# Optimization experiments

Measured on AMD Instinct MI355X. Metric: run time of the kernel, lower is better.

Reference implementation:

```python
import jax, jax.numpy as jnp
import numpy as np

NUM_HEAD = 16
D_Q = 512
D_KV = 512
ROPE_BASE = 10000.0


def _cos_sin(seq_len, dim):
    # Replicates calculate_cos_sin: theta = base**(-2*ids) / (dim//2)
    pos = jnp.arange(seq_len, dtype=jnp.float32)[:, None]          # (S,1)
    ids = jnp.arange(dim // 2, dtype=jnp.float32)                  # (D/2,)
    theta = (ROPE_BASE ** (-2.0 * ids)) / (dim // 2)
    r = pos * theta[None, :]                                       # (S, D/2)
    return jnp.cos(r), jnp.sin(r)


def _rope(x, cos, sin):
    b, s, d = x.shape
    xv = x.reshape(b, s, d // 2, 2)
    x0, x1 = xv[..., 0], xv[..., 1]
    out = jnp.stack([x0 * cos - x1 * sin, x1 * cos + x0 * sin], axis=-1)
    return out.reshape(b, s, d)


def setup_inputs() -> dict:
    key = jax.random.key(0)
    ks = jax.random.split(key, 10)
    d_model, d_q, d_kv = 1024, D_Q, D_KV
    b, s = 2, 2048
    w = lambda k, i, o: jax.random.normal(k, (i, o), dtype=jnp.float32) * 0.02
    return {
        "x": jax.random.normal(ks[0], (b, s, d_model), dtype=jnp.float32),
        "Wd_q_w": w(ks[1], d_model, d_q), "Wd_q_b": jnp.zeros((d_q,), jnp.float32),
        "Wu_q_w": w(ks[2], d_q, d_model), "Wu_q_b": jnp.zeros((d_model,), jnp.float32),
        "Wq_r_w": w(ks[3], d_q, d_model), "Wq_r_b": jnp.zeros((d_model,), jnp.float32),
        "Wk_r_w": w(ks[4], d_model, d_model), "Wk_r_b": jnp.zeros((d_model,), jnp.float32),
        "Wd_kv_w": w(ks[5], d_model, d_kv), "Wd_kv_b": jnp.zeros((d_kv,), jnp.float32),
        "Wu_k_w": w(ks[6], d_kv, d_model), "Wu_k_b": jnp.zeros((d_model,), jnp.float32),
        "Wu_v_w": w(ks[7], d_kv, d_model), "Wu_v_b": jnp.zeros((d_model,), jnp.float32),
        "Wo_w": w(ks[8], d_model, d_model), "Wo_b": jnp.zeros((d_model,), jnp.float32),
    }


def reference(x, Wd_q_w, Wd_q_b, Wu_q_w, Wu_q_b, Wq_r_w, Wq_r_b,
              Wk_r_w, Wk_r_b, Wd_kv_w, Wd_kv_b, Wu_k_w, Wu_k_b,
              Wu_v_w, Wu_v_b, Wo_w, Wo_b):
    b, s, d_model = x.shape
    h = NUM_HEAD
    hd = d_model // h
    scale = jnp.sqrt(jnp.float32(h + D_KV + D_Q))

    def heads(t):  # (b,s,d) -> (b,h,s,hd)
        return t.reshape(b, s, h, hd).transpose(0, 2, 1, 3)

    cos, sin = _cos_sin(s, d_model)

    ct_q = x @ Wd_q_w + Wd_q_b                                   # (b,s,d_q)
    qt_c = heads(ct_q @ Wu_q_w + Wu_q_b)
    qt_r = heads(_rope(ct_q @ Wq_r_w + Wq_r_b, cos, sin))
    query = qt_c + qt_r                                          # (b,h,s,hd)

    ct_kv = x @ Wd_kv_w + Wd_kv_b                                # (b,s,d_kv)
    kt_c = heads(ct_kv @ Wu_k_w + Wu_k_b)
    kt_r = heads(_rope(x @ Wk_r_w + Wk_r_b, cos, sin))
    key = kt_c + kt_r
    value = heads(ct_kv @ Wu_v_w + Wu_v_b)

    attn = jnp.einsum('bhqd,bhkd->bhqk', query, key) / scale
    attn = jax.nn.softmax(attn, axis=-1)
    out = jnp.einsum('bhqk,bhkd->bhqd', attn, value)
    out = out.transpose(0, 2, 1, 3).reshape(b, s, d_model)
    return out @ Wo_w + Wo_b
```

## Files before the change

### kernel.cpp

```cpp
#include <hip/hip_runtime.h>
#include <hip/hip_bf16.h>
#include <math.h>
#include <limits.h>

typedef __hip_bfloat16 bf16;
typedef __bf16 bf16x8 __attribute__((ext_vector_type(8)));
typedef float  f32x4  __attribute__((ext_vector_type(4)));

#define DEVI __device__ __forceinline__

static constexpr int Bb     = 2;
static constexpr int Ss     = 2048;
static constexpr int DMODEL = 1024;
static constexpr int NTOK   = Bb * Ss;

DEVI float bf2f(bf16 v) { return __bfloat162float(v); }
DEVI bf16  f2bf(float v) { return __float2bfloat16(v); }

DEVI unsigned int packbf(float lo, float hi) {
  union { bf16 b; unsigned short u; } a, c;
  a.b = f2bf(lo); c.b = f2bf(hi);
  return ((unsigned int)c.u << 16) | a.u;
}
DEVI float bfu2f(unsigned short u) {
  unsigned int x = (unsigned int)u << 16;
  float f; __builtin_memcpy(&f, &x, 4); return f;
}

DEVI void async_load16(const bf16* g, bf16* l) {
  __builtin_amdgcn_global_load_lds((const __attribute__((address_space(1))) void*)g,
                                   (__attribute__((address_space(3))) void*)l, 16, 0, 0);
}

__global__ __launch_bounds__(256) void convert_kernel(
    const float* __restrict__ in, bf16* __restrict__ out, int n4) {
  const int t = blockIdx.x * blockDim.x + threadIdx.x;
  if (t >= n4) return;
  const float4 v = ((const float4*)in)[t];
  uint2 o; o.x = packbf(v.x, v.y); o.y = packbf(v.z, v.w);
  *(uint2*)&out[(size_t)t * 4] = o;
}

struct TransDesc { const float* src; bf16* dst; int R; int C; int tstart; };
struct TransPack { TransDesc d[8]; };

__global__ __launch_bounds__(256) void transpose8_kernel(TransPack p) {
  const int t = blockIdx.x;
  int i = 0;
#pragma unroll
  for (int j = 1; j < 8; ++j) if (t >= p.d[j].tstart) i = j;
  const float* __restrict__ in = p.d[i].src;
  bf16* __restrict__ out = p.d[i].dst;
  const int R = p.d[i].R, C = p.d[i].C;
  const int rel = t - p.d[i].tstart;
  const int tilesC = C >> 6;
  const int r0 = (rel / tilesC) * 64, c0 = (rel % tilesC) * 64;

  __shared__ bf16 tl[64][65];
  const int tc = threadIdx.x & 63, tr = threadIdx.x >> 6;
#pragma unroll
  for (int q = 0; q < 16; ++q) {
    int r = tr + q * 4;
    tl[r][tc] = f2bf(in[(size_t)(r0 + r) * C + c0 + tc]);
  }
  __syncthreads();
#pragma unroll
  for (int q = 0; q < 16; ++q) {
    int r = tr + q * 4;
    out[(size_t)(c0 + r) * R + r0 + tc] = tl[tc][r];
  }
}

struct GemmDesc {
  const bf16* A; const bf16* WT; const float* b1; const float* b2; bf16* C;
  int lda, ldb, ldc, K, bsplit, nTX, blkStart, biasRow;
};
struct GemmBatch { GemmDesc d[4]; };

__global__ __launch_bounds__(256) void gemm_batch_kernel(GemmBatch gb) {
  const int t = blockIdx.x;
  int di = 0;
#pragma unroll
  for (int j = 1; j < 4; ++j) if (t >= gb.d[j].blkStart) di = j;
  const GemmDesc D = gb.d[di];
  const int rel = t - D.blkStart;
  const int tileN = (rel % D.nTX) * 128;
  const int tileM = (rel / D.nTX) * 128;

  __shared__ bf16 ldsA[128 * 32];
  __shared__ bf16 ldsB[128 * 32];
  const int tid = threadIdx.x;
  const int lane = tid & 63;
  const int w = tid >> 6;
  const int wr = w >> 1, wc = w & 1;
  const int l15 = lane & 15, lg = lane >> 4;
  const int lrow = lane >> 2;
  const int lcol = (lane & 3) * 8;

  f32x4 acc[4][4] = {};

  for (int k0 = 0; k0 < D.K; k0 += 32) {
    async_load16(D.A  + (size_t)(tileM + w * 32 +      lrow) * D.lda + k0 + lcol, &ldsA[(w * 32) * 32]);
    async_load16(D.A  + (size_t)(tileM + w * 32 + 16 + lrow) * D.lda + k0 + lcol, &ldsA[(w * 32 + 16) * 32]);
    async_load16(D.WT + (size_t)(tileN + w * 32 +      lrow) * D.ldb + k0 + lcol, &ldsB[(w * 32) * 32]);
    async_load16(D.WT + (size_t)(tileN + w * 32 + 16 + lrow) * D.ldb + k0 + lcol, &ldsB[(w * 32 + 16) * 32]);
    __syncthreads();

    bf16x8 af[4], bfr[4];
#pragma unroll
    for (int i = 0; i < 4; ++i) {
      af[i]  = *(const bf16x8*)&ldsA[(wr * 64 + i * 16 + l15) * 32 + lg * 8];
      bfr[i] = *(const bf16x8*)&ldsB[(wc * 64 + i * 16 + l15) * 32 + lg * 8];
    }
#pragma unroll
    for (int i = 0; i < 4; ++i)
#pragma unroll
      for (int j = 0; j < 4; ++j)
        acc[i][j] = __builtin_amdgcn_mfma_f32_16x16x32_bf16(af[i], bfr[j], acc[i][j], 0, 0, 0);
    __syncthreads();
  }

  const int mbase = tileM + wr * 64;
  const int nbase = tileN + wc * 64;
#pragma unroll
  for (int j = 0; j < 4; ++j) {
    int col = nbase + j * 16 + l15;
    float bvc = D.biasRow ? 0.0f : (col < D.bsplit ? D.b1[col] : D.b2[col - D.bsplit]);
#pragma unroll
    for (int i = 0; i < 4; ++i)
#pragma unroll
      for (int r = 0; r < 4; ++r) {
        int row = mbase + i * 16 + lg * 4 + r;
        float bv = D.biasRow ? D.b1[row] : bvc;
        D.C[(size_t)row * D.ldc + col] = f2bf(acc[i][j][r] + bv);
      }
  }
}

__global__ __launch_bounds__(256) void gemm_kernel_f32(
    const bf16* __restrict__ A, int lda,
    const bf16* __restrict__ WT, int ldb,
    const float* __restrict__ b1,
    float* __restrict__ Cout, int ldc, int K) {
  __shared__ bf16 ldsA[128 * 32];
  __shared__ bf16 ldsB[128 * 32];
  const int tid = threadIdx.x;
  const int lane = tid & 63;
  const int w = tid >> 6;
  const int wr = w >> 1, wc = w & 1;
  const int tileM = blockIdx.y * 128;
  const int tileN = blockIdx.x * 128;
  const int l15 = lane & 15, lg = lane >> 4;
  const int lrow = lane >> 2;
  const int lcol = (lane & 3) * 8;

  f32x4 acc[4][4] = {};

  for (int k0 = 0; k0 < K; k0 += 32) {
    async_load16(A  + (size_t)(tileM + w * 32 +      lrow) * lda + k0 + lcol, &ldsA[(w * 32) * 32]);
    async_load16(A  + (size_t)(tileM + w * 32 + 16 + lrow) * lda + k0 + lcol, &ldsA[(w * 32 + 16) * 32]);
    async_load16(WT + (size_t)(tileN + w * 32 +      lrow) * ldb + k0 + lcol, &ldsB[(w * 32) * 32]);
    async_load16(WT + (size_t)(tileN + w * 32 + 16 + lrow) * ldb + k0 + lcol, &ldsB[(w * 32 + 16) * 32]);
    __syncthreads();

    bf16x8 af[4], bfr[4];
#pragma unroll
    for (int i = 0; i < 4; ++i) {
      af[i]  = *(const bf16x8*)&ldsA[(wr * 64 + i * 16 + l15) * 32 + lg * 8];
      bfr[i] = *(const bf16x8*)&ldsB[(wc * 64 + i * 16 + l15) * 32 + lg * 8];
    }
#pragma unroll
    for (int i = 0; i < 4; ++i)
#pragma unroll
      for (int j = 0; j < 4; ++j)
        acc[i][j] = __builtin_amdgcn_mfma_f32_16x16x32_bf16(af[i], bfr[j], acc[i][j], 0, 0, 0);
    __syncthreads();
  }

  const int mbase = tileM + wr * 64;
  const int nbase = tileN + wc * 64;
#pragma unroll
  for (int j = 0; j < 4; ++j) {
    int col = nbase + j * 16 + l15;
    float bvc = b1[col];
#pragma unroll
    for (int i = 0; i < 4; ++i)
#pragma unroll
      for (int r = 0; r < 4; ++r) {
        int row = mbase + i * 16 + lg * 4 + r;
        Cout[(size_t)row * ldc + col] = acc[i][j][r] + bvc;
      }
  }
}

__global__ __launch_bounds__(256) void combine_rope_kernel(
    const bf16* __restrict__ Gc, int ldc_,
    const bf16* __restrict__ Gr, int ldr_,
    bf16* __restrict__ out) {
  const int t = blockIdx.x * blockDim.x + threadIdx.x;
  const int g = t & 127, row = t >> 7;
  const int s = row & (Ss - 1);
  union { bf16x8 v; unsigned short u[8]; } vc, vr;
  vc.v = *(const bf16x8*)&Gc[(size_t)row * ldc_ + (size_t)g * 8];
  vr.v = *(const bf16x8*)&Gr[(size_t)row * ldr_ + (size_t)g * 8];
  uint4 o;
  unsigned int* op = &o.x;
#pragma unroll
  for (int qq = 0; qq < 4; ++qq) {
    const int p = g * 4 + qq;
    float c, sn;
    if (p == 0) {
      float rr = (float)s * (1.0f / 512.0f);
      c = cosf(rr); sn = sinf(rr);
    } else {
      float theta = exp2f(-26.5754247590989f * (float)p) * (1.0f / 512.0f);
      sn = (float)s * theta; c = 1.0f;
    }
    float g0 = bfu2f(vr.u[2 * qq]), g1 = bfu2f(vr.u[2 * qq + 1]);
    float c0 = bfu2f(vc.u[2 * qq]), c1 = bfu2f(vc.u[2 * qq + 1]);
    op[qq] = packbf(c0 + g0 * c - g1 * sn, c1 + g1 * c + g0 * sn);
  }
  *(uint4*)&out[(size_t)row * DMODEL + (size_t)g * 8] = o;
}

__global__ __launch_bounds__(256) void attn_kernel(
    const bf16* __restrict__ Qn, const bf16* __restrict__ Kn,
    const bf16* __restrict__ VT, bf16* __restrict__ AO) {
  const int bh = blockIdx.x, qt = blockIdx.y;
  const int b = bh >> 4, h = bh & 15;
  const int tid = threadIdx.x, lane = tid & 63, w = tid >> 6;
  const int q0 = qt * 64 + w * 16;
  const int l15 = lane & 15, lg = lane >> 4;
  const float SC2 = 0.044736075f;
  const float THR = 11.5415603f;

  __shared__ bf16 ldsK[2][64 * 64];
  __shared__ bf16 ldsV[2][64 * 64];
  __shared__ bf16 ldsP[4][16 * 64];

  const bf16* Kg = Kn + (size_t)(b * Ss) * DMODEL + h * 64;
  const bf16* Vg = VT + (size_t)(h * 64) * NTOK + b * Ss;

  const int r0 = tid >> 3;
  const int srcb = ((tid & 7) * 16) ^ ((r0 & 7) << 4);
  const char* kS0 = (const char*)(Kg + (size_t)r0 * DMODEL) + srcb;
  const char* kS1 = (const char*)(Kg + (size_t)(32 + r0) * DMODEL) + srcb;
  const char* vS0 = (const char*)(Vg + (size_t)r0 * NTOK) + srcb;
  const char* vS1 = (const char*)(Vg + (size_t)(32 + r0) * NTOK) + srcb;
  const ptrdiff_t kAdv = (ptrdiff_t)64 * DMODEL * 2;
  const ptrdiff_t vAdv = 128;

  bf16* kd0_b0 = &ldsK[0][w * 512]; bf16* kd1_b0 = &ldsK[0][2048 + w * 512];
  bf16* kd0_b1 = &ldsK[1][w * 512]; bf16* kd1_b1 = &ldsK[1][2048 + w * 512];
  bf16* vd0_b0 = &ldsV[0][w * 512]; bf16* vd1_b0 = &ldsV[0][2048 + w * 512];
  bf16* vd0_b1 = &ldsV[1][w * 512]; bf16* vd1_b1 = &ldsV[1][2048 + w * 512];

  auto stageTo = [&](bf16* kd0, bf16* kd1, bf16* vd0, bf16* vd1) {
    async_load16((const bf16*)kS0, kd0);
    async_load16((const bf16*)kS1, kd1);
    async_load16((const bf16*)vS0, vd0);
    async_load16((const bf16*)vS1, vd1);
    kS0 += kAdv; kS1 += kAdv; vS0 += vAdv; vS1 += vAdv;
  };

  const int kswz = (l15 & 7) << 4;
  const int xA = (lg * 16) ^ kswz;
  const int xB = (64 + lg * 16) ^ kswz;
  const char* krA0 = (const char*)&ldsK[0][0] + l15 * 128 + xA;
  const char* krB0 = (const char*)&ldsK[0][0] + l15 * 128 + xB;
  const char* krA1 = (const char*)&ldsK[1][0] + l15 * 128 + xA;
  const char* krB1 = (const char*)&ldsK[1][0] + l15 * 128 + xB;
  const char* vrA0 = (const char*)&ldsV[0][0] + l15 * 128 + xA;
  const char* vrB0 = (const char*)&ldsV[0][0] + l15 * 128 + xB;
  const char* vrA1 = (const char*)&ldsV[1][0] + l15 * 128 + xA;
  const char* vrB1 = (const char*)&ldsV[1][0] + l15 * 128 + xB;

  char* Pw = (char*)&ldsP[w][0];
  char* pwr[4];
#pragma unroll
  for (int j = 0; j < 4; ++j) {
    const int chunk = (j * 2 + (lg >> 1)) ^ (l15 & 7);
    pwr[j] = Pw + l15 * 128 + chunk * 16 + (lg & 1) * 8;
  }
  const char* paA = Pw + l15 * 128 + xA;
  const char* paB = Pw + l15 * 128 + xB;

  const bf16* Qbase = Qn + (size_t)(b * Ss + q0 + l15) * DMODEL + h * 64;
  bf16x8 bq0 = *(const bf16x8*)&Qbase[lg * 8];
  bf16x8 bq1 = *(const bf16x8*)&Qbase[32 + lg * 8];

  float m = 0.0f, l = 0.0f;
  f32x4 accO[4] = {};

  auto body = [&](const char* krA, const char* krB, const char* vrA, const char* vrB) {
    f32x4 sa[4] = {};
#pragma unroll
    for (int j = 0; j < 4; ++j) {
      bf16x8 ak0 = *(const bf16x8*)(krA + j * 2048);
      bf16x8 ak1 = *(const bf16x8*)(krB + j * 2048);
      sa[j] = __builtin_amdgcn_mfma_f32_16x16x32_bf16(ak0, bq0, sa[j], 0, 0, 0);
      sa[j] = __builtin_amdgcn_mfma_f32_16x16x32_bf16(ak1, bq1, sa[j], 0, 0, 0);
    }
    float pmaxr = -3.0e38f;
#pragma unroll
    for (int j = 0; j < 4; ++j)
#pragma unroll
      for (int r = 0; r < 4; ++r) pmaxr = fmaxf(pmaxr, sa[j][r]);
    if (__any(fmaf(pmaxr, SC2, -m) > THR)) {
      float px = fmaxf(pmaxr, __shfl_xor(pmaxr, 16, 64));
      px = fmaxf(px, __shfl_xor(px, 32, 64));
      float mnew = fmaxf(m, px * SC2);
      float corr = __builtin_amdgcn_exp2f(m - mnew);
      m = mnew; l *= corr;
      float cr[4];
#pragma unroll
      for (int r = 0; r < 4; ++r) cr[r] = __shfl(corr, lg * 4 + r, 64);
#pragma unroll
      for (int dj = 0; dj < 4; ++dj)
#pragma unroll
        for (int r = 0; r < 4; ++r) accO[dj][r] *= cr[r];
    }
    float p[4][4];
    float ts0 = 0.f, ts1 = 0.f;
#pragma unroll
    for (int j = 0; j < 4; ++j) {
#pragma unroll
      for (int r = 0; r < 4; ++r)
        p[j][r] = __builtin_amdgcn_exp2f(fmaf(sa[j][r], SC2, -m));
      ts0 += p[j][0] + p[j][2];
      ts1 += p[j][1] + p[j][3];
    }
    float ts = ts0 + ts1;
    ts += __shfl_xor(ts, 16, 64);
    ts += __shfl_xor(ts, 32, 64);
    l += ts;
#pragma unroll
    for (int j = 0; j < 4; ++j) {
      uint2 pw;
      pw.x = packbf(p[j][0], p[j][1]);
      pw.y = packbf(p[j][2], p[j][3]);
      *(uint2*)pwr[j] = pw;
    }
    bf16x8 pa0 = *(const bf16x8*)paA;
    bf16x8 pa1 = *(const bf16x8*)paB;
#pragma unroll
    for (int dj = 0; dj < 4; ++dj) {
      bf16x8 bv0 = *(const bf16x8*)(vrA + dj * 2048);
      bf16x8 bv1 = *(const bf16x8*)(vrB + dj * 2048);
      accO[dj] = __builtin_amdgcn_mfma_f32_16x16x32_bf16(pa0, bv0, accO[dj], 0, 0, 0);
      accO[dj] = __builtin_amdgcn_mfma_f32_16x16x32_bf16(pa1, bv1, accO[dj], 0, 0, 0);
    }
  };

  stageTo(kd0_b0, kd1_b0, vd0_b0, vd1_b0);
  for (int tt = 0; tt < 16; ++tt) {
    __syncthreads();
    stageTo(kd0_b1, kd1_b1, vd0_b1, vd1_b1);
    body(krA0, krB0, vrA0, vrB0);
    __syncthreads();
    if (tt < 15) stageTo(kd0_b0, kd1_b0, vd0_b0, vd1_b0);
    body(krA1, krB1, vrA1, vrB1);
  }

  float linv[4];
#pragma unroll
  for (int r = 0; r < 4; ++r) linv[r] = 1.0f / __shfl(l, lg * 4 + r, 64);
#pragma unroll
  for (int dj = 0; dj < 4; ++dj)
#pragma unroll
    for (int r = 0; r < 4; ++r)
      AO[(size_t)(b * Ss + q0 + lg * 4 + r) * DMODEL + h * 64 + dj * 16 + l15] =
          f2bf(accO[dj][r] * linv[r]);
}

extern "C" void kernel_launch(void* const* d_in, const int* in_sizes, int n_in,
                              void* d_out, int out_size, void* d_ws, size_t ws_size,
                              hipStream_t stream) {
  const float* x      = (const float*)d_in[0];
  const float* Wdq    = (const float*)d_in[1];  const float* Wdq_b  = (const float*)d_in[2];
  const float* Wuq    = (const float*)d_in[3];  const float* Wuq_b  = (const float*)d_in[4];
  const float* Wqr    = (const float*)d_in[5];  const float* Wqr_b  = (const float*)d_in[6];
  const float* Wkr    = (const float*)d_in[7];  const float* Wkr_b  = (const float*)d_in[8];
  const float* Wdkv   = (const float*)d_in[9];  const float* Wdkv_b = (const float*)d_in[10];
  const float* Wuk    = (const float*)d_in[11]; const float* Wuk_b  = (const float*)d_in[12];
  const float* Wuv    = (const float*)d_in[13]; const float* Wuv_b  = (const float*)d_in[14];
  const float* Wo     = (const float*)d_in[15]; const float* Wo_b   = (const float*)d_in[16];

  char* ws = (char*)d_ws;
  size_t off = 0;
  bf16* WdqT   = (bf16*)(ws + off); off += (size_t)512  * 1024 * 2;
  bf16* WdkvT  = (bf16*)(ws + off); off += (size_t)512  * 1024 * 2;
  bf16* WuqT   = (bf16*)(ws + off); off += (size_t)1024 * 512  * 2;
  bf16* WqrT   = (bf16*)(ws + off); off += (size_t)1024 * 512  * 2;
  bf16* WukT   = (bf16*)(ws + off); off += (size_t)1024 * 512  * 2;
  bf16* WuvT   = (bf16*)(ws + off); off += (size_t)1024 * 512  * 2;
  bf16* WkrT   = (bf16*)(ws + off); off += (size_t)1024 * 1024 * 2;
  bf16* WoT    = (bf16*)(ws + off); off += (size_t)1024 * 1024 * 2;
  bf16* x_bf   = (bf16*)(ws + off); off += (size_t)NTOK * 1024 * 2;
  bf16* ct     = (bf16*)(ws + off); off += (size_t)NTOK * 1024 * 2;
  bf16* Ga     = (bf16*)(ws + off); off += (size_t)NTOK * 1024 * 2;
  bf16* VTr    = (bf16*)(ws + off); off += (size_t)NTOK * 1024 * 2;
  bf16* Gupk   = x_bf;
  bf16* Qn     = (bf16*)d_out;
  bf16* Kn     = (bf16*)d_out + (size_t)NTOK * DMODEL;
  bf16* AO     = Ga;
  (void)ws_size; (void)in_sizes; (void)n_in; (void)out_size;

  TransPack tp = {{
    { Wdq,  WdqT,  1024, 512,  0    },
    { Wdkv, WdkvT, 1024, 512,  128  },
    { Wuq,  WuqT,  512,  1024, 256  },
    { Wqr,  WqrT,  512,  1024, 384  },
    { Wuk,  WukT,  512,  1024, 512  },
    { Wuv,  WuvT,  512,  1024, 640  },
    { Wkr,  WkrT,  1024, 1024, 768  },
    { Wo,   WoT,   1024, 1024, 1024 },
  }};
  transpose8_kernel<<<1280, 256, 0, stream>>>(tp);
  convert_kernel<<<(NTOK * DMODEL / 4 + 255) / 256, 256, 0, stream>>>(x, x_bf, NTOK * DMODEL / 4);

  GemmBatch ba = {{
    { x_bf, WdqT, Wdq_b, Wdkv_b, ct, 1024, 1024, 1024, 1024, 512,     8, 0,       0 },
    { x_bf, WkrT, Wkr_b, Wkr_b,  Kn, 1024, 1024, 1024, 1024, INT_MAX, 8, 256,     0 },
    { 0, 0, 0, 0, 0, 0, 0, 0, 0, 0, 1, INT_MAX, 0 },
    { 0, 0, 0, 0, 0, 0, 0, 0, 0, 0, 1, INT_MAX, 0 },
  }};
  gemm_batch_kernel<<<512, 256, 0, stream>>>(ba);

  GemmBatch bb = {{
    { ct,       WuqT,     Wuq_b, Wuq_b, Ga,   1024, 512,  1024, 512, INT_MAX, 8,  0,   0 },
    { ct,       WqrT,     Wqr_b, Wqr_b, Qn,   1024, 512,  1024, 512, INT_MAX, 8,  256, 0 },
    { ct + 512, WukT,     Wuk_b, Wuk_b, Gupk, 1024, 512,  1024, 512, INT_MAX, 8,  512, 0 },
    { WuvT,     ct + 512, Wuv_b, Wuv_b, VTr,  512,  1024, NTOK, 512, INT_MAX, 32, 768, 1 },
  }};
  gemm_batch_kernel<<<1024, 256, 0, stream>>>(bb);

  combine_rope_kernel<<<NTOK * 128 / 256, 256, 0, stream>>>(Ga, 1024, Qn, 1024, Qn);
  combine_rope_kernel<<<NTOK * 128 / 256, 256, 0, stream>>>(Gupk, 1024, Kn, 1024, Kn);

  attn_kernel<<<dim3(32, 32), 256, 0, stream>>>(Qn, Kn, VTr, AO);

  gemm_kernel_f32<<<dim3(8, 32), 256, 0, stream>>>(
      AO, 1024, WoT, 1024, Wo_b, (float*)d_out, 1024, 1024);
}
```

Before: 197.4 us.

## Precompose low-rank projection weights and replace RoPE combine with rank-2 fixup

The down- and up-projections are multiplied together on device into full 1024x1024 matrices, and their biases are folded in. Q, K and V then each come from a single GEMM on x, replacing the two-stage low-rank chain and the separate x@Wkr GEMM. K's rotary term is added through a new addend path in the GEMM epilogue. The elementwise combine/RoPE passes are replaced by a small fixup kernel that only corrects the first rotary pair, since the other frequencies are negligible. This cuts main-GEMM FLOPs and intermediate traffic, at the cost of extra weight-composition GEMMs, a prep kernel and different bf16 rounding paths.

After: 297.7 us. +50.8%, slower.

```diff
diff --git a/kernel.cpp b/kernel.cpp
--- a/kernel.cpp
+++ b/kernel.cpp
@@ -22,26 +22,28 @@
   a.b = f2bf(lo); c.b = f2bf(hi);
   return ((unsigned int)c.u << 16) | a.u;
 }
-DEVI float bfu2f(unsigned short u) {
-  unsigned int x = (unsigned int)u << 16;
-  float f; __builtin_memcpy(&f, &x, 4); return f;
-}
 
 DEVI void async_load16(const bf16* g, bf16* l) {
   __builtin_amdgcn_global_load_lds((const __attribute__((address_space(1))) void*)g,
                                    (__attribute__((address_space(3))) void*)l, 16, 0, 0);
 }
 
-__global__ __launch_bounds__(256) void convert_kernel(
-    const float* __restrict__ in, bf16* __restrict__ out, int n4) {
-  const int t = blockIdx.x * blockDim.x + threadIdx.x;
-  if (t >= n4) return;
+__global__ __launch_bounds__(256) void convert3_kernel(
+    const float* __restrict__ i0, bf16* __restrict__ o0, int n0,
+    const float* __restrict__ i1, bf16* __restrict__ o1, int n1,
+    const float* __restrict__ i2, bf16* __restrict__ o2, int n2) {
+  int t = blockIdx.x * blockDim.x + threadIdx.x;
+  const float* in; bf16* out;
+  if (t < n0)           { in = i0; out = o0; }
+  else if (t < n0 + n1) { t -= n0; in = i1; out = o1; }
+  else if (t < n0 + n1 + n2) { t -= n0 + n1; in = i2; out = o2; }
+  else return;
   const float4 v = ((const float4*)in)[t];
   uint2 o; o.x = packbf(v.x, v.y); o.y = packbf(v.z, v.w);
   *(uint2*)&out[(size_t)t * 4] = o;
 }
 
-struct TransDesc { const float* src; bf16* dst; int R; int C; int tstart; };
+struct TransDesc { const float* src; const float* src2; bf16* dst; int R; int C; int tstart; };
 struct TransPack { TransDesc d[8]; };
 
 __global__ __launch_bounds__(256) void transpose8_kernel(TransPack p) {
@@ -49,7 +51,8 @@
   int i = 0;
 #pragma unroll
   for (int j = 1; j < 8; ++j) if (t >= p.d[j].tstart) i = j;
-  const float* __restrict__ in = p.d[i].src;
+  const float* __restrict__ in  = p.d[i].src;
+  const float* __restrict__ in2 = p.d[i].src2;
   bf16* __restrict__ out = p.d[i].dst;
   const int R = p.d[i].R, C = p.d[i].C;
   const int rel = t - p.d[i].tstart;
@@ -61,7 +64,9 @@
 #pragma unroll
   for (int q = 0; q < 16; ++q) {
     int r = tr + q * 4;
-    tl[r][tc] = f2bf(in[(size_t)(r0 + r) * C + c0 + tc]);
+    float v = in[(size_t)(r0 + r) * C + c0 + tc];
+    if (in2) v += in2[(size_t)(r0 + r) * C + c0 + tc];
+    tl[r][tc] = f2bf(v);
   }
   __syncthreads();
 #pragma unroll
@@ -71,9 +76,50 @@
   }
 }
 
+__global__ __launch_bounds__(256) void prep_kernel(
+    const float* __restrict__ Wdq, const float* __restrict__ Wuq, const float* __restrict__ Wqr,
+    const float* __restrict__ Wuk, const float* __restrict__ Wuv, const float* __restrict__ Wkr,
+    const float* __restrict__ Wdq_b, const float* __restrict__ Wuq_b, const float* __restrict__ Wqr_b,
+    const float* __restrict__ Wdkv_b, const float* __restrict__ Wuk_b, const float* __restrict__ Wkr_b,
+    const float* __restrict__ Wuv_b,
+    float* __restrict__ qb, float* __restrict__ kb, float* __restrict__ vb,
+    float* __restrict__ mqr01, float* __restrict__ wkr01, float* __restrict__ fixb,
+    float* __restrict__ zb) {
+  const int t = blockIdx.x * blockDim.x + threadIdx.x;
+  if (t < 1024) {
+    const int j = t;
+    float a = 0.f, bsum = 0.f, c = 0.f;
+    for (int cc = 0; cc < 512; ++cc) {
+      float w1 = Wdq_b[cc], w2 = Wdkv_b[cc];
+      a    += w1 * (Wuq[(size_t)cc * 1024 + j] + Wqr[(size_t)cc * 1024 + j]);
+      bsum += w2 * Wuk[(size_t)cc * 1024 + j];
+      c    += w2 * Wuv[(size_t)cc * 1024 + j];
+    }
+    qb[j] = a + Wuq_b[j] + Wqr_b[j];
+    kb[j] = bsum + Wuk_b[j] + Wkr_b[j];
+    vb[j] = c + Wuv_b[j];
+    zb[j] = 0.f;
+  } else if (t < 3072) {
+    const int idx = t - 1024, i = idx >> 1, tt = idx & 1;
+    float s = 0.f;
+    for (int cc = 0; cc < 512; ++cc) s += Wdq[(size_t)i * 512 + cc] * Wqr[(size_t)cc * 1024 + tt];
+    mqr01[idx] = s;
+    wkr01[idx] = Wkr[(size_t)i * 1024 + tt];
+  } else if (t < 3076) {
+    const int tt = t - 3072;
+    if (tt < 2) {
+      float s = 0.f;
+      for (int cc = 0; cc < 512; ++cc) s += Wdq_b[cc] * Wqr[(size_t)cc * 1024 + tt];
+      fixb[tt] = s + Wqr_b[tt];
+    } else {
+      fixb[tt] = Wkr_b[tt - 2];
+    }
+  }
+}
+
 struct GemmDesc {
-  const bf16* A; const bf16* WT; const float* b1; const float* b2; bf16* C;
-  int lda, ldb, ldc, K, bsplit, nTX, blkStart, biasRow;
+  const bf16* A; const bf16* WT; const float* b1; const float* b2; const bf16* addm; bf16* C;
+  int lda, ldb, ldc, ldadd, K, bsplit, nTX, blkStart, biasRow;
 };
 struct GemmBatch { GemmDesc d[4]; };
 
@@ -132,7 +178,9 @@
       for (int r = 0; r < 4; ++r) {
         int row = mbase + i * 16 + lg * 4 + r;
         float bv = D.biasRow ? D.b1[row] : bvc;
-        D.C[(size_t)row * D.ldc + col] = f2bf(acc[i][j][r] + bv);
+        float v = acc[i][j][r] + bv;
+        if (D.addm) v += bf2f(D.addm[(size_t)row * D.ldadd + col]);
+        D.C[(size_t)row * D.ldc + col] = f2bf(v);
       }
   }
 }
@@ -193,34 +241,42 @@
   }
 }
 
-__global__ __launch_bounds__(256) void combine_rope_kernel(
-    const bf16* __restrict__ Gc, int ldc_,
-    const bf16* __restrict__ Gr, int ldr_,
-    bf16* __restrict__ out) {
-  const int t = blockIdx.x * blockDim.x + threadIdx.x;
-  const int g = t & 127, row = t >> 7;
-  const int s = row & (Ss - 1);
-  union { bf16x8 v; unsigned short u[8]; } vc, vr;
-  vc.v = *(const bf16x8*)&Gc[(size_t)row * ldc_ + (size_t)g * 8];
-  vr.v = *(const bf16x8*)&Gr[(size_t)row * ldr_ + (size_t)g * 8];
-  uint4 o;
-  unsigned int* op = &o.x;
-#pragma unroll
-  for (int qq = 0; qq < 4; ++qq) {
-    const int p = g * 4 + qq;
-    float c, sn;
-    if (p == 0) {
-      float rr = (float)s * (1.0f / 512.0f);
-      c = cosf(rr); sn = sinf(rr);
-    } else {
-      float theta = exp2f(-26.5754247590989f * (float)p) * (1.0f / 512.0f);
-      sn = (float)s * theta; c = 1.0f;
-    }
-    float g0 = bfu2f(vr.u[2 * qq]), g1 = bfu2f(vr.u[2 * qq + 1]);
-    float c0 = bfu2f(vc.u[2 * qq]), c1 = bfu2f(vc.u[2 * qq + 1]);
-    op[qq] = packbf(c0 + g0 * c - g1 * sn, c1 + g1 * c + g0 * sn);
-  }
-  *(uint4*)&out[(size_t)row * DMODEL + (size_t)g * 8] = o;
+__global__ __launch_bounds__(256) void fixup_kernel(
+    const bf16* __restrict__ x_bf, const float* __restrict__ mqr01,
+    const float* __restrict__ wkr01, const float* __restrict__ fixb,
+    bf16* __restrict__ Qn, bf16* __restrict__ Kn) {
+  const int row = blockIdx.x * 4 + (threadIdx.x >> 6);
+  const int lane = threadIdx.x & 63;
+  float q0 = 0.f, q1 = 0.f, k0 = 0.f, k1 = 0.f;
+  const bf16* xr = x_bf + (size_t)row * DMODEL + lane * 16;
+  const float* mq = mqr01 + lane * 32;
+  const float* mk = wkr01 + lane * 32;
+#pragma unroll
+  for (int e = 0; e < 16; ++e) {
+    float xv = bf2f(xr[e]);
+    q0 = fmaf(xv, mq[e * 2 + 0], q0);
+    q1 = fmaf(xv, mq[e * 2 + 1], q1);
+    k0 = fmaf(xv, mk[e * 2 + 0], k0);
+    k1 = fmaf(xv, mk[e * 2 + 1], k1);
+  }
+#pragma unroll
+  for (int d = 32; d >= 1; d >>= 1) {
+    q0 += __shfl_xor(q0, d, 64);
+    q1 += __shfl_xor(q1, d, 64);
+    k0 += __shfl_xor(k0, d, 64);
+    k1 += __shfl_xor(k1, d, 64);
+  }
+  if (lane == 0) {
+    const float rr = (float)(row & (Ss - 1)) * (1.0f / 512.0f);
+    const float c = cosf(rr) - 1.0f, sn = sinf(rr);
+    const float qr0 = q0 + fixb[0], qr1 = q1 + fixb[1];
+    const float kr0 = k0 + fixb[2], kr1 = k1 + fixb[3];
+    const size_t base = (size_t)row * DMODEL;
+    Qn[base]     = f2bf(bf2f(Qn[base])     + qr0 * c - qr1 * sn);
+    Qn[base + 1] = f2bf(bf2f(Qn[base + 1]) + qr1 * c + qr0 * sn);
+    Kn[base]     = f2bf(bf2f(Kn[base])     + kr0 * c - kr1 * sn);
+    Kn[base + 1] = f2bf(bf2f(Kn[base + 1]) + kr1 * c + kr0 * sn);
+  }
 }
 
 __global__ __launch_bounds__(256) void attn_kernel(
@@ -388,55 +444,65 @@
 
   char* ws = (char*)d_ws;
   size_t off = 0;
-  bf16* WdqT   = (bf16*)(ws + off); off += (size_t)512  * 1024 * 2;
-  bf16* WdkvT  = (bf16*)(ws + off); off += (size_t)512  * 1024 * 2;
-  bf16* WuqT   = (bf16*)(ws + off); off += (size_t)1024 * 512  * 2;
-  bf16* WqrT   = (bf16*)(ws + off); off += (size_t)1024 * 512  * 2;
+  bf16* WuqqrT = (bf16*)(ws + off); off += (size_t)1024 * 512  * 2;
   bf16* WukT   = (bf16*)(ws + off); off += (size_t)1024 * 512  * 2;
   bf16* WuvT   = (bf16*)(ws + off); off += (size_t)1024 * 512  * 2;
   bf16* WkrT   = (bf16*)(ws + off); off += (size_t)1024 * 1024 * 2;
   bf16* WoT    = (bf16*)(ws + off); off += (size_t)1024 * 1024 * 2;
+  bf16* Wdq_bf = (bf16*)(ws + off); off += (size_t)1024 * 512  * 2;
+  bf16* Wdkv_bf= (bf16*)(ws + off); off += (size_t)1024 * 512  * 2;
   bf16* x_bf   = (bf16*)(ws + off); off += (size_t)NTOK * 1024 * 2;
-  bf16* ct     = (bf16*)(ws + off); off += (size_t)NTOK * 1024 * 2;
-  bf16* Ga     = (bf16*)(ws + off); off += (size_t)NTOK * 1024 * 2;
+  bf16* MqT    = (bf16*)(ws + off); off += (size_t)1024 * 1024 * 2;
+  bf16* MkT    = (bf16*)(ws + off); off += (size_t)1024 * 1024 * 2;
+  bf16* MvT    = (bf16*)(ws + off); off += (size_t)1024 * 1024 * 2;
   bf16* VTr    = (bf16*)(ws + off); off += (size_t)NTOK * 1024 * 2;
-  bf16* Gupk   = x_bf;
+  bf16* AO     = (bf16*)(ws + off); off += (size_t)NTOK * 1024 * 2;
+  float* qb    = (float*)(ws + off); off += 1024 * 4;
+  float* kb    = (float*)(ws + off); off += 1024 * 4;
+  float* vb    = (float*)(ws + off); off += 1024 * 4;
+  float* zb    = (float*)(ws + off); off += 1024 * 4;
+  float* mqr01 = (float*)(ws + off); off += 2048 * 4;
+  float* wkr01 = (float*)(ws + off); off += 2048 * 4;
+  float* fixb  = (float*)(ws + off); off += 4 * 4;
   bf16* Qn     = (bf16*)d_out;
   bf16* Kn     = (bf16*)d_out + (size_t)NTOK * DMODEL;
-  bf16* AO     = Ga;
   (void)ws_size; (void)in_sizes; (void)n_in; (void)out_size;
 
+  const int nx = NTOK * DMODEL / 4, nw = 1024 * 512 / 4;
+  convert3_kernel<<<(nx + 2 * nw + 255) / 256, 256, 0, stream>>>(
+      x, x_bf, nx, Wdq, Wdq_bf, nw, Wdkv, Wdkv_bf, nw);
+
   TransPack tp = {{
-    { Wdq,  WdqT,  1024, 512,  0    },
-    { Wdkv, WdkvT, 1024, 512,  128  },
-    { Wuq,  WuqT,  512,  1024, 256  },
-    { Wqr,  WqrT,  512,  1024, 384  },
-    { Wuk,  WukT,  512,  1024, 512  },
-    { Wuv,  WuvT,  512,  1024, 640  },
-    { Wkr,  WkrT,  1024, 1024, 768  },
-    { Wo,   WoT,   1024, 1024, 1024 },
+    { Wuq, Wqr,  WuqqrT, 512,  1024, 0        },
+    { Wuk, 0,    WukT,   512,  1024, 128      },
+    { Wuv, 0,    WuvT,   512,  1024, 256      },
+    { Wkr, 0,    WkrT,   1024, 1024, 384      },
+    { Wo,  0,    WoT,    1024, 1024, 640      },
+    { 0, 0, 0, 0, 0, 1 << 30 }, { 0, 0, 0, 0, 0, 1 << 30 }, { 0, 0, 0, 0, 0, 1 << 30 },
   }};
-  transpose8_kernel<<<1280, 256, 0, stream>>>(tp);
-  convert_kernel<<<(NTOK * DMODEL / 4 + 255) / 256, 256, 0, stream>>>(x, x_bf, NTOK * DMODEL / 4);
-
-  GemmBatch ba = {{
-    { x_bf, WdqT, Wdq_b, Wdkv_b, ct, 1024, 1024, 1024, 1024, 512,     8, 0,       0 },
-    { x_bf, WkrT, Wkr_b, Wkr_b,  Kn, 1024, 1024, 1024, 1024, INT_MAX, 8, 256,     0 },
-    { 0, 0, 0, 0, 0, 0, 0, 0, 0, 0, 1, INT_MAX, 0 },
-    { 0, 0, 0, 0, 0, 0, 0, 0, 0, 0, 1, INT_MAX, 0 },
+  transpose8_kernel<<<896, 256, 0, stream>>>(tp);
+
+  prep_kernel<<<13, 256, 0, stream>>>(Wdq, Wuq, Wqr, Wuk, Wuv, Wkr,
+                                      Wdq_b, Wuq_b, Wqr_b, Wdkv_b, Wuk_b, Wkr_b, Wuv_b,
+                                      qb, kb, vb, mqr01, wkr01, fixb, zb);
+
+  GemmBatch fb = {{
+    { WuqqrT, Wdq_bf,  zb, zb, 0,    MqT, 512, 512, 1024, 0,    512, INT_MAX, 8, 0,       0 },
+    { WukT,   Wdkv_bf, zb, zb, WkrT, MkT, 512, 512, 1024, 1024, 512, INT_MAX, 8, 64,      0 },
+    { WuvT,   Wdkv_bf, zb, zb, 0,    MvT, 512, 512, 1024, 0,    512, INT_MAX, 8, 128,     0 },
+    { 0, 0, 0, 0, 0, 0, 0, 0, 0, 0, 0, 0, 1, 1 << 30, 0 },
   }};
-  gemm_batch_kernel<<<512, 256, 0, stream>>>(ba);
-
-  GemmBatch bb = {{
-    { ct,       WuqT,     Wuq_b, Wuq_b, Ga,   1024, 512,  1024, 512, INT_MAX, 8,  0,   0 },
-    { ct,       WqrT,     Wqr_b, Wqr_b, Qn,   1024, 512,  1024, 512, INT_MAX, 8,  256, 0 },
-    { ct + 512, WukT,     Wuk_b, Wuk_b, Gupk, 1024, 512,  1024, 512, INT_MAX, 8,  512, 0 },
-    { WuvT,     ct + 512, Wuv_b, Wuv_b, VTr,  512,  1024, NTOK, 512, INT_MAX, 32, 768, 1 },
+  gemm_batch_kernel<<<192, 256, 0, stream>>>(fb);
+
+  GemmBatch mb = {{
+    { x_bf, MqT,  qb, qb, 0, Qn,  1024, 1024, 1024, 0, 1024, INT_MAX, 8,  0,       0 },
+    { x_bf, MkT,  kb, kb, 0, Kn,  1024, 1024, 1024, 0, 1024, INT_MAX, 8,  256,     0 },
+    { MvT,  x_bf, vb, vb, 0, VTr, 1024, 1024, NTOK, 0, 1024, INT_MAX, 32, 512,     1 },
+    { 0, 0, 0, 0, 0, 0, 0, 0, 0, 0, 0, 0, 1, 1 << 30, 0 },
   }};
-  gemm_batch_kernel<<<1024, 256, 0, stream>>>(bb);
-
-  combine_rope_kernel<<<NTOK * 128 / 256, 256, 0, stream>>>(Ga, 1024, Qn, 1024, Qn);
-  combine_rope_kernel<<<NTOK * 128 / 256, 256, 0, stream>>>(Gupk, 1024, Kn, 1024, Kn);
+  gemm_batch_kernel<<<768, 256, 0, stream>>>(mb);
+
+  fixup_kernel<<<NTOK / 4, 256, 0, stream>>>(x_bf, mqr01, wkr01, fixb, Qn, Kn);
 
   attn_kernel<<<dim3(32, 32), 256, 0, stream>>>(Qn, Kn, VTr, AO);
 
```
